# Optimization experiments

Hardware: AMD Instinct MI355X
Metric: run time of the kernel (lower is better)

The kernel has to match this reference:

```python
import jax, jax.numpy as jnp
import numpy as np

N, E, G = 2000, 8000, 100          # nodes, edges, graphs
F_NODE, F_EDGE, H, FC = 22, 4, 128, 64
EPS = 1e-5                          # BatchNorm eps (eval mode, running stats)


def setup_inputs() -> dict:
    key = jax.random.key(0)
    ks = jax.random.split(key, 24)
    rn = lambda k, s, sc=0.1: jax.random.normal(k, s, jnp.float32) * sc
    inp = {}
    inp["x"] = jax.random.normal(ks[0], (N, F_NODE), jnp.float32)
    inp["edge_index"] = jax.random.randint(ks[1], (2, E), 0, N, jnp.int64)
    inp["edge_attr"] = jax.random.uniform(ks[2], (E, F_EDGE), jnp.float32)
    inp["batch"] = jnp.sort(jax.random.randint(ks[3], (N,), 0, G, jnp.int64))
    # edge networks (Linear + ReLU) producing per-edge weight matrices
    inp["We1"] = rn(ks[4], (F_EDGE, F_NODE * H)); inp["be1"] = jnp.zeros((F_NODE * H,), jnp.float32)
    inp["We2"] = rn(ks[5], (F_EDGE, H * H));      inp["be2"] = jnp.zeros((H * H,), jnp.float32)
    inp["We3"] = rn(ks[6], (F_EDGE, H * H));      inp["be3"] = jnp.zeros((H * H,), jnp.float32)
    # NNConv root weights + biases
    inp["Wr1"] = rn(ks[7], (F_NODE, H)); inp["br1"] = jnp.zeros((H,), jnp.float32)
    inp["Wr2"] = rn(ks[8], (H, H));      inp["br2"] = jnp.zeros((H,), jnp.float32)
    inp["Wr3"] = rn(ks[9], (H, H));      inp["br3"] = jnp.zeros((H,), jnp.float32)
    # BatchNorm (eval): gamma, beta, running_mean, running_var
    for i, k in zip((1, 2, 3), (ks[10], ks[11], ks[12])):
        inp[f"g{i}"] = 1.0 + rn(k, (H,), 0.05)
        inp[f"b{i}"] = jnp.zeros((H,), jnp.float32)
        inp[f"rm{i}"] = jnp.zeros((H,), jnp.float32)
        inp[f"rv{i}"] = jnp.ones((H,), jnp.float32)
    # head MLP
    inp["Wf1"] = rn(ks[13], (H, FC)); inp["bf1"] = jnp.zeros((FC,), jnp.float32)
    inp["Wf2"] = rn(ks[14], (FC, 1)); inp["bf2"] = jnp.zeros((1,), jnp.float32)
    return inp


def _nnconv(x, src, dst, edge_attr, We, be, Wr, br, din, dout):
    # per-edge weight matrix from edge features: [E, din, dout]
    w = jax.nn.relu(edge_attr @ We + be).reshape(-1, din, dout)
    msg = jnp.einsum('ei,eio->eo', x[src], w)          # gather + batched matvec
    agg = jax.ops.segment_sum(msg, dst, num_segments=N)  # scatter-add at targets
    return agg + x @ Wr + br                            # root transform + bias


def _bn(x, g, b, rm, rv):
    return (x - rm) * jax.lax.rsqrt(rv + EPS) * g + b


def reference(x, edge_index, edge_attr, batch,
              We1, be1, We2, be2, We3, be3,
              Wr1, br1, Wr2, br2, Wr3, br3,
              g1, b1, rm1, rv1, g2, b2, rm2, rv2, g3, b3, rm3, rv3,
              Wf1, bf1, Wf2, bf2):
    src, dst = edge_index[0], edge_index[1]
    h = jax.nn.relu(_bn(_nnconv(x, src, dst, edge_attr, We1, be1, Wr1, br1, F_NODE, H), g1, b1, rm1, rv1))
    h = jax.nn.relu(_bn(_nnconv(h, src, dst, edge_attr, We2, be2, Wr2, br2, H, H), g2, b2, rm2, rv2))
    h = jax.nn.relu(_bn(_nnconv(h, src, dst, edge_attr, We3, be3, Wr3, br3, H, H), g3, b3, rm3, rv3))
    # global mean pool over graphs
    sums = jax.ops.segment_sum(h, batch, num_segments=G)
    cnts = jax.ops.segment_sum(jnp.ones((N,), h.dtype), batch, num_segments=G)
    pooled = sums / jnp.maximum(cnts, 1.0)[:, None]
    # head MLP (dropout is identity at inference)
    out = jax.nn.relu(pooled @ Wf1 + bf1) @ Wf2 + bf2
    return out  # [G, 1]
```

## Files before the change

### kernel.cpp

```cpp
#include <hip/hip_runtime.h>
#include <hip/hip_bf16.h>
#include <math.h>

#define N_NODES 2000
#define N_EDGES 8000
#define N_GRAPH 100
#define F_NODE 22
#define F_EDGE 4
#define H 128
#define FC 64
#define EPSBN 1e-5f
#define EPB 16
#define EPT 8

#define C2 (H * H)
#define NEB (N_EDGES / EPB)

#define MSG1_B NEB
#define ROOT1_B (N_NODES / 8)
#define PRE_TOTAL (2 * C2 + 2 * 4096 + 3 * H)
#define PRE_B ((PRE_TOTAL + 255) / 256)
#define GRID1 (MSG1_B + ROOT1_B + PRE_B)

#define MSGH_B (NEB * 2)
#define ROOTH_B (N_NODES / 8)
#define GRID23 (MSGH_B + ROOTH_B)


#define COMP_CHUNK(WREG, BREG, BASE)                                           \
  {                                                                            \
    float bu_[4] = {BREG.x, BREG.y, BREG.z, BREG.w};                           \
    _Pragma("unroll")                                                          \
    for (int u = 0; u < 4; u++) {                                              \
      float4 xa_ = *(const float4*)&xs[(BASE) + u][eh * EPT];                  \
      float4 xb_ = *(const float4*)&xs[(BASE) + u][eh * EPT + 4];              \
      float xq_[8] = {xa_.x, xa_.y, xa_.z, xa_.w, xb_.x, xb_.y, xb_.z, xb_.w}; \
      float4 wv_ = WREG[u];                                                    \
      _Pragma("unroll")                                                        \
      for (int q = 0; q < 8; q++) {                                            \
        float w_ = fmaf(wv_.x, ear[q][0], bu_[u]);                             \
        w_ = fmaf(wv_.y, ear[q][1], w_);                                       \
        w_ = fmaf(wv_.z, ear[q][2], w_);                                       \
        w_ = fmaf(wv_.w, ear[q][3], w_);                                       \
        w_ = fmaxf(w_, 0.f);                                                   \
        acc[q] = fmaf(xq_[q], w_, acc[q]);                                     \
      }                                                                        \
    }                                                                          \
  }

__device__ __forceinline__ void msg_body_H(
    const float* __restrict__ xin, const int* __restrict__ ei,
    const float* __restrict__ ea, const float4* __restrict__ Wp,
    const float4* __restrict__ bp4, const float* __restrict__ ABp,
    float* __restrict__ agg, int mblk)
{
    __shared__ float xs[64][EPB];
    __shared__ float eas[EPB][4];
    __shared__ int dsts[EPB];
    const int eb = mblk % NEB;
    const int I0 = (mblk / NEB) * 64;
    const int e0 = eb * EPB;
    const int tid = threadIdx.x;

    if (tid < EPB * 4) { int e = tid >> 2, k = tid & 3; eas[e][k] = ea[(e0 + e) * 4 + k]; }
    if (tid >= 64 && tid < 64 + EPB) dsts[tid - 64] = ei[N_EDGES + e0 + (tid - 64)];
    for (int idx = tid; idx < EPB * 64; idx += 256) {
        int i = idx >> 4, e = idx & 15;
        int s = ei[e0 + e];
        float v = xin[s * H + I0 + i];
        xs[i][e] = fmaxf(fmaf(v, ABp[I0 + i], ABp[H + I0 + i]), 0.f);
    }
    __syncthreads();

    const int o = tid & 127;
    const int eh = tid >> 7;

    float ear[EPT][4], acc[EPT];
#pragma unroll
    for (int q = 0; q < EPT; q++) {
        acc[q] = 0.f;
#pragma unroll
        for (int k = 0; k < 4; k++) ear[q][k] = eas[eh * EPT + q][k];
    }

    const float4* wp = Wp + I0 * H + o;
    const float4* bp = bp4 + (I0 / 4) * H + o;

    float4 wA[4], wB[4], bA, bB;
#pragma unroll
    for (int u = 0; u < 4; u++) wA[u] = wp[u * H];
    bA = bp[0];

#pragma unroll 1
    for (int ii = 0; ii < 64; ii += 8) {
#pragma unroll
        for (int u = 0; u < 4; u++) wB[u] = wp[(ii + 4 + u) * H];
        bB = bp[(ii / 4 + 1) * H];
        COMP_CHUNK(wA, bA, ii)
        if (ii + 8 < 64) {
#pragma unroll
            for (int u = 0; u < 4; u++) wA[u] = wp[(ii + 8 + u) * H];
            bA = bp[(ii / 4 + 2) * H];
        }
        COMP_CHUNK(wB, bB, ii + 4)
    }

#pragma unroll
    for (int q = 0; q < EPT; q++)
        atomicAdd(&agg[dsts[eh * EPT + q] * H + o], acc[q]);
}

__device__ __forceinline__ void msg_body_1(
    const float* __restrict__ xin, const int* __restrict__ ei,
    const float* __restrict__ ea, const float* __restrict__ We1,
    const float* __restrict__ be1, float* __restrict__ agg, int mblk)
{
    __shared__ float xs[24][EPB];
    __shared__ float eas[EPB][4];
    __shared__ int dsts[EPB];
    const int e0 = mblk * EPB;
    const int tid = threadIdx.x;

    if (tid < EPB * 4) { int e = tid >> 2, k = tid & 3; eas[e][k] = ea[(e0 + e) * 4 + k]; }
    if (tid >= 64 && tid < 64 + EPB) dsts[tid - 64] = ei[N_EDGES + e0 + (tid - 64)];
    for (int idx = tid; idx < EPB * 24; idx += 256) {
        int i = idx >> 4, e = idx & 15;
        int s = ei[e0 + e];
        xs[i][e] = (i < F_NODE) ? xin[s * F_NODE + i] : 0.f;
    }
    __syncthreads();

    const int o = tid & 127;
    const int eh = tid >> 7;

    float ear[EPT][4], acc[EPT];
#pragma unroll
    for (int q = 0; q < EPT; q++) {
        acc[q] = 0.f;
#pragma unroll
        for (int k = 0; k < 4; k++) ear[q][k] = eas[eh * EPT + q][k];
    }

    for (int ii = 0; ii < 24; ii += 4) {
        float4 w4[4]; float bb[4];
#pragma unroll
        for (int u = 0; u < 4; u++) {
            int row = ii + u;
            if (row < F_NODE) {
                w4[u] = make_float4(We1[0 * (F_NODE * H) + row * H + o],
                                    We1[1 * (F_NODE * H) + row * H + o],
                                    We1[2 * (F_NODE * H) + row * H + o],
                                    We1[3 * (F_NODE * H) + row * H + o]);
                bb[u] = be1[row * H + o];
            } else { w4[u] = make_float4(0.f, 0.f, 0.f, 0.f); bb[u] = 0.f; }
        }
#pragma unroll
        for (int u = 0; u < 4; u++) {
            float4 xa = *(const float4*)&xs[ii + u][eh * EPT];
            float4 xb = *(const float4*)&xs[ii + u][eh * EPT + 4];
            float xq[8] = {xa.x, xa.y, xa.z, xa.w, xb.x, xb.y, xb.z, xb.w};
            float4 wv = w4[u];
#pragma unroll
            for (int q = 0; q < 8; q++) {
                float w = fmaf(wv.x, ear[q][0], bb[u]);
                w = fmaf(wv.y, ear[q][1], w);
                w = fmaf(wv.z, ear[q][2], w);
                w = fmaf(wv.w, ear[q][3], w);
                w = fmaxf(w, 0.f);
                acc[q] = fmaf(xq[q], w, acc[q]);
            }
        }
    }

#pragma unroll
    for (int q = 0; q < EPT; q++)
        atomicAdd(&agg[dsts[eh * EPT + q] * H + o], acc[q]);
}

template <int DIN, bool ACT>
__device__ __forceinline__ void root_body(
    const float* __restrict__ hin, const float4* __restrict__ Wr4,
    const float4* __restrict__ br4, const float* __restrict__ ABp,
    float* __restrict__ agg, int rblk)
{
    constexpr int NPB = 8;
    __shared__ float hs[NPB][DIN];
    const int n0 = rblk * NPB;
    const int tid = threadIdx.x;
    for (int idx = tid; idx < NPB * DIN; idx += 256) {
        int nl = idx / DIN, i = idx - nl * DIN;
        float v = hin[(n0 + nl) * DIN + i];
        if (ACT) v = fmaxf(fmaf(v, ABp[i], ABp[H + i]), 0.f);
        hs[nl][i] = v;
    }
    __syncthreads();
    const int og = tid & 31;
    const int nl = tid >> 5;
    float4 acc = br4[og];
#pragma unroll 4
    for (int i = 0; i < DIN; i++) {
        float4 w = Wr4[i * (H / 4) + og];
        float xv = hs[nl][i];
        acc.x = fmaf(xv, w.x, acc.x);
        acc.y = fmaf(xv, w.y, acc.y);
        acc.z = fmaf(xv, w.z, acc.z);
        acc.w = fmaf(xv, w.w, acc.w);
    }
    float* dst = agg + (n0 + nl) * H + og * 4;
    atomicAdd(dst + 0, acc.x);
    atomicAdd(dst + 1, acc.y);
    atomicAdd(dst + 2, acc.z);
    atomicAdd(dst + 3, acc.w);
}

__device__ __forceinline__ void pre_body(
    const float* __restrict__ We2, const float* __restrict__ be2,
    const float* __restrict__ We3, const float* __restrict__ be3,
    const float* __restrict__ g1, const float* __restrict__ b1,
    const float* __restrict__ rm1, const float* __restrict__ rv1,
    const float* __restrict__ g2, const float* __restrict__ b2,
    const float* __restrict__ rm2, const float* __restrict__ rv2,
    const float* __restrict__ g3, const float* __restrict__ b3,
    const float* __restrict__ rm3, const float* __restrict__ rv3,
    float4* __restrict__ We2p, float4* __restrict__ We3p,
    float4* __restrict__ be2p4, float4* __restrict__ be3p4,
    float* __restrict__ AB, int pblk)
{
    int t = pblk * 256 + threadIdx.x;
    if (t < C2) {
        We2p[t] = make_float4(We2[t], We2[C2 + t], We2[2 * C2 + t], We2[3 * C2 + t]);
        return;
    }
    t -= C2;
    if (t < C2) {
        We3p[t] = make_float4(We3[t], We3[C2 + t], We3[2 * C2 + t], We3[3 * C2 + t]);
        return;
    }
    t -= C2;
    if (t < 4096) {
        int c = t / H, o = t - c * H;
        be2p4[t] = make_float4(be2[(4 * c) * H + o], be2[(4 * c + 1) * H + o],
                               be2[(4 * c + 2) * H + o], be2[(4 * c + 3) * H + o]);
        return;
    }
    t -= 4096;
    if (t < 4096) {
        int c = t / H, o = t - c * H;
        be3p4[t] = make_float4(be3[(4 * c) * H + o], be3[(4 * c + 1) * H + o],
                               be3[(4 * c + 2) * H + o], be3[(4 * c + 3) * H + o]);
        return;
    }
    t -= 4096;
    if (t < 3 * H) {
        int l = t / H, o = t - l * H;
        const float *g, *b, *rm, *rv;
        if (l == 0) { g = g1; b = b1; rm = rm1; rv = rv1; }
        else if (l == 1) { g = g2; b = b2; rm = rm2; rv = rv2; }
        else { g = g3; b = b3; rm = rm3; rv = rv3; }
        float A = g[o] * rsqrtf(rv[o] + EPSBN);
        AB[l * 2 * H + o] = A;
        AB[l * 2 * H + H + o] = b[o] - rm[o] * A;
    }
}

__global__ __launch_bounds__(256) void stage1_kernel(
    const float* x, const int* ei, const float* ea,
    const float* We1, const float* be1,
    const float4* Wr1_4, const float4* br1_4,
    const float* We2, const float* be2, const float* We3, const float* be3,
    const float* g1, const float* b1, const float* rm1, const float* rv1,
    const float* g2, const float* b2, const float* rm2, const float* rv2,
    const float* g3, const float* b3, const float* rm3, const float* rv3,
    float4* We2p, float4* We3p, float4* be2p4, float4* be3p4, float* AB,
    float* h1)
{
    const int b = blockIdx.x;
    if (b < MSG1_B) {
        msg_body_1(x, ei, ea, We1, be1, h1, b);
    } else if (b < MSG1_B + ROOT1_B) {
        root_body<F_NODE, false>(x, Wr1_4, br1_4, nullptr, h1, b - MSG1_B);
    } else {
        pre_body(We2, be2, We3, be3,
                 g1, b1, rm1, rv1, g2, b2, rm2, rv2, g3, b3, rm3, rv3,
                 We2p, We3p, be2p4, be3p4, AB, b - MSG1_B - ROOT1_B);
    }
}

__global__ __launch_bounds__(256) void layer_kernel(
    const float* hin, const int* ei, const float* ea,
    const float4* Wp, const float4* bp4,
    const float4* Wr4, const float4* br4,
    const float* ABprev, float* hout)
{
    const int b = blockIdx.x;
    if (b < MSGH_B) {
        msg_body_H(hin, ei, ea, Wp, bp4, ABprev, hout, b);
    } else {
        root_body<H, true>(hin, Wr4, br4, ABprev, hout, b - MSGH_B);
    }
}

__global__ __launch_bounds__(128) void pool_head_kernel(
    const float* __restrict__ h, const int* __restrict__ batch,
    const float* __restrict__ AB,
    const float* __restrict__ Wf1, const float* __restrict__ bf1,
    const float* __restrict__ Wf2, const float* __restrict__ bf2,
    float* __restrict__ out)
{
    __shared__ float pooled[H];
    const int g = blockIdx.x;
    const int t = threadIdx.x;

    int a = 0, b = N_NODES;
    while (a < b) { int m = (a + b) >> 1; if (batch[m] < g) a = m + 1; else b = m; }
    const int lo = a;
    b = N_NODES;
    while (a < b) { int m = (a + b) >> 1; if (batch[m] < g + 1) a = m + 1; else b = m; }
    const int hi = a;

    float s = 0.f;
    const float Ao = AB[t], Bo = AB[H + t];
    for (int n = lo; n < hi; n++) {
        float v = h[n * H + t];
        s += fmaxf(fmaf(v, Ao, Bo), 0.f);
    }
    pooled[t] = (hi > lo) ? s / (float)(hi - lo) : 0.f;
    __syncthreads();

    if (t < FC) {
        float f = bf1[t];
#pragma unroll 4
        for (int i = 0; i < H; i++) f = fmaf(pooled[i], Wf1[i * FC + t], f);
        f = fmaxf(f, 0.f);
        float p = f * Wf2[t];
#pragma unroll
        for (int off = 32; off; off >>= 1) p += __shfl_down(p, off);
        if (t == 0) out[g] = p + bf2[0];
    }
}

extern "C" void kernel_launch(void* const* d_in, const int* in_sizes, int n_in,
                              void* d_out, int out_size, void* d_ws, size_t ws_size,
                              hipStream_t stream) {
    const float* x   = (const float*)d_in[0];
    const int* ei    = (const int*)d_in[1];
    const float* ea  = (const float*)d_in[2];
    const int* batch = (const int*)d_in[3];
    const float* We1 = (const float*)d_in[4];
    const float* be1 = (const float*)d_in[5];
    const float* We2 = (const float*)d_in[6];
    const float* be2 = (const float*)d_in[7];
    const float* We3 = (const float*)d_in[8];
    const float* be3 = (const float*)d_in[9];
    const float* Wr1 = (const float*)d_in[10];
    const float* br1 = (const float*)d_in[11];
    const float* Wr2 = (const float*)d_in[12];
    const float* br2 = (const float*)d_in[13];
    const float* Wr3 = (const float*)d_in[14];
    const float* br3 = (const float*)d_in[15];
    const float* g1 = (const float*)d_in[16], *b1 = (const float*)d_in[17];
    const float* rm1 = (const float*)d_in[18], *rv1 = (const float*)d_in[19];
    const float* g2 = (const float*)d_in[20], *b2 = (const float*)d_in[21];
    const float* rm2 = (const float*)d_in[22], *rv2 = (const float*)d_in[23];
    const float* g3 = (const float*)d_in[24], *b3 = (const float*)d_in[25];
    const float* rm3 = (const float*)d_in[26], *rv3 = (const float*)d_in[27];
    const float* Wf1 = (const float*)d_in[28];
    const float* bf1 = (const float*)d_in[29];
    const float* Wf2 = (const float*)d_in[30];
    const float* bf2 = (const float*)d_in[31];

    float* out = (float*)d_out;

    float* ws = (float*)d_ws;
    float* h1    = ws;
    float* h2    = h1 + N_NODES * H;
    float* h3    = h2 + N_NODES * H;
    float* We2p  = h3 + N_NODES * H;
    float* We3p  = We2p + C2 * 4;
    float* be2p4 = We3p + C2 * 4;
    float* be3p4 = be2p4 + 4096 * 4;
    float* AB    = be3p4 + 4096 * 4;

    stage1_kernel<<<GRID1, 256, 0, stream>>>(
        x, ei, ea, We1, be1,
        (const float4*)Wr1, (const float4*)br1,
        We2, be2, We3, be3,
        g1, b1, rm1, rv1, g2, b2, rm2, rv2, g3, b3, rm3, rv3,
        (float4*)We2p, (float4*)We3p, (float4*)be2p4, (float4*)be3p4, AB,
        h1);

    layer_kernel<<<GRID23, 256, 0, stream>>>(
        h1, ei, ea, (const float4*)We2p, (const float4*)be2p4,
        (const float4*)Wr2, (const float4*)br2, AB + 0 * 2 * H, h2);

    layer_kernel<<<GRID23, 256, 0, stream>>>(
        h2, ei, ea, (const float4*)We3p, (const float4*)be3p4,
        (const float4*)Wr3, (const float4*)br3, AB + 1 * 2 * H, h3);

    pool_head_kernel<<<N_GRAPH, 128, 0, stream>>>(
        h3, batch, AB + 2 * 2 * H, Wf1, bf1, Wf2, bf2, out);
}
```

Baseline: 200.3 us.

## Fuse all stages into one cooperative persistent kernel with grid syncs

Replaces the four sequential kernel launches with a single cooperative persistent kernel that loops over work units per phase and separates phases with grid-wide syncs. The goal is to remove launch overhead and inter-kernel gaps, which are significant for a workload of only a few hundred microseconds. The grid is capped by occupancy times CU count, so blocks may process several units in series. The per-call host occupancy and attribute queries add CPU overhead, and a fallback path keeps the old multi-kernel launch sequence.

```diff
diff --git a/kernel.cpp b/kernel.cpp
--- a/kernel.cpp
+++ b/kernel.cpp
@@ -1,6 +1,9 @@
 #include <hip/hip_runtime.h>
+#include <hip/hip_cooperative_groups.h>
 #include <hip/hip_bf16.h>
 #include <math.h>
+
+namespace cg = cooperative_groups;
 
 #define N_NODES 2000
 #define N_EDGES 8000
@@ -20,11 +23,11 @@
 #define ROOT1_B (N_NODES / 8)
 #define PRE_TOTAL (2 * C2 + 2 * 4096 + 3 * H)
 #define PRE_B ((PRE_TOTAL + 255) / 256)
-#define GRID1 (MSG1_B + ROOT1_B + PRE_B)
+#define PHA_U (MSG1_B + ROOT1_B + PRE_B)
 
 #define MSGH_B (NEB * 2)
 #define ROOTH_B (N_NODES / 8)
-#define GRID23 (MSGH_B + ROOTH_B)
+#define PHB_U (MSGH_B + ROOTH_B)
 
 
 #define COMP_CHUNK(WREG, BREG, BASE)                                           \
@@ -115,18 +118,18 @@
     const float* __restrict__ ea, const float* __restrict__ We1,
     const float* __restrict__ be1, float* __restrict__ agg, int mblk)
 {
-    __shared__ float xs[24][EPB];
-    __shared__ float eas[EPB][4];
-    __shared__ int dsts[EPB];
+    __shared__ float xs1[24][EPB];
+    __shared__ float eas1[EPB][4];
+    __shared__ int dsts1[EPB];
     const int e0 = mblk * EPB;
     const int tid = threadIdx.x;
 
-    if (tid < EPB * 4) { int e = tid >> 2, k = tid & 3; eas[e][k] = ea[(e0 + e) * 4 + k]; }
-    if (tid >= 64 && tid < 64 + EPB) dsts[tid - 64] = ei[N_EDGES + e0 + (tid - 64)];
+    if (tid < EPB * 4) { int e = tid >> 2, k = tid & 3; eas1[e][k] = ea[(e0 + e) * 4 + k]; }
+    if (tid >= 64 && tid < 64 + EPB) dsts1[tid - 64] = ei[N_EDGES + e0 + (tid - 64)];
     for (int idx = tid; idx < EPB * 24; idx += 256) {
         int i = idx >> 4, e = idx & 15;
         int s = ei[e0 + e];
-        xs[i][e] = (i < F_NODE) ? xin[s * F_NODE + i] : 0.f;
+        xs1[i][e] = (i < F_NODE) ? xin[s * F_NODE + i] : 0.f;
     }
     __syncthreads();
 
@@ -138,7 +141,7 @@
     for (int q = 0; q < EPT; q++) {
         acc[q] = 0.f;
 #pragma unroll
-        for (int k = 0; k < 4; k++) ear[q][k] = eas[eh * EPT + q][k];
+        for (int k = 0; k < 4; k++) ear[q][k] = eas1[eh * EPT + q][k];
     }
 
     for (int ii = 0; ii < 24; ii += 4) {
@@ -156,8 +159,8 @@
         }
 #pragma unroll
         for (int u = 0; u < 4; u++) {
-            float4 xa = *(const float4*)&xs[ii + u][eh * EPT];
-            float4 xb = *(const float4*)&xs[ii + u][eh * EPT + 4];
+            float4 xa = *(const float4*)&xs1[ii + u][eh * EPT];
+            float4 xb = *(const float4*)&xs1[ii + u][eh * EPT + 4];
             float xq[8] = {xa.x, xa.y, xa.z, xa.w, xb.x, xb.y, xb.z, xb.w};
             float4 wv = w4[u];
 #pragma unroll
@@ -174,7 +177,7 @@
 
 #pragma unroll
     for (int q = 0; q < EPT; q++)
-        atomicAdd(&agg[dsts[eh * EPT + q] * H + o], acc[q]);
+        atomicAdd(&agg[dsts1[eh * EPT + q] * H + o], acc[q]);
 }
 
 template <int DIN, bool ACT>
@@ -263,52 +266,14 @@
     }
 }
 
-__global__ __launch_bounds__(256) void stage1_kernel(
-    const float* x, const int* ei, const float* ea,
-    const float* We1, const float* be1,
-    const float4* Wr1_4, const float4* br1_4,
-    const float* We2, const float* be2, const float* We3, const float* be3,
-    const float* g1, const float* b1, const float* rm1, const float* rv1,
-    const float* g2, const float* b2, const float* rm2, const float* rv2,
-    const float* g3, const float* b3, const float* rm3, const float* rv3,
-    float4* We2p, float4* We3p, float4* be2p4, float4* be3p4, float* AB,
-    float* h1)
-{
-    const int b = blockIdx.x;
-    if (b < MSG1_B) {
-        msg_body_1(x, ei, ea, We1, be1, h1, b);
-    } else if (b < MSG1_B + ROOT1_B) {
-        root_body<F_NODE, false>(x, Wr1_4, br1_4, nullptr, h1, b - MSG1_B);
-    } else {
-        pre_body(We2, be2, We3, be3,
-                 g1, b1, rm1, rv1, g2, b2, rm2, rv2, g3, b3, rm3, rv3,
-                 We2p, We3p, be2p4, be3p4, AB, b - MSG1_B - ROOT1_B);
-    }
-}
-
-__global__ __launch_bounds__(256) void layer_kernel(
-    const float* hin, const int* ei, const float* ea,
-    const float4* Wp, const float4* bp4,
-    const float4* Wr4, const float4* br4,
-    const float* ABprev, float* hout)
-{
-    const int b = blockIdx.x;
-    if (b < MSGH_B) {
-        msg_body_H(hin, ei, ea, Wp, bp4, ABprev, hout, b);
-    } else {
-        root_body<H, true>(hin, Wr4, br4, ABprev, hout, b - MSGH_B);
-    }
-}
-
-__global__ __launch_bounds__(128) void pool_head_kernel(
+__device__ __forceinline__ void pool_head_body(
     const float* __restrict__ h, const int* __restrict__ batch,
     const float* __restrict__ AB,
     const float* __restrict__ Wf1, const float* __restrict__ bf1,
     const float* __restrict__ Wf2, const float* __restrict__ bf2,
-    float* __restrict__ out)
+    float* __restrict__ out, int g)
 {
     __shared__ float pooled[H];
-    const int g = blockIdx.x;
     const int t = threadIdx.x;
 
     int a = 0, b = N_NODES;
@@ -318,13 +283,15 @@
     while (a < b) { int m = (a + b) >> 1; if (batch[m] < g + 1) a = m + 1; else b = m; }
     const int hi = a;
 
-    float s = 0.f;
-    const float Ao = AB[t], Bo = AB[H + t];
-    for (int n = lo; n < hi; n++) {
-        float v = h[n * H + t];
-        s += fmaxf(fmaf(v, Ao, Bo), 0.f);
-    }
-    pooled[t] = (hi > lo) ? s / (float)(hi - lo) : 0.f;
+    if (t < H) {
+        float s = 0.f;
+        const float Ao = AB[t], Bo = AB[H + t];
+        for (int n = lo; n < hi; n++) {
+            float v = h[n * H + t];
+            s += fmaxf(fmaf(v, Ao, Bo), 0.f);
+        }
+        pooled[t] = (hi > lo) ? s / (float)(hi - lo) : 0.f;
+    }
     __syncthreads();
 
     if (t < FC) {
@@ -339,38 +306,119 @@
     }
 }
 
+struct KArgs {
+    const float *x; const int *ei; const float *ea; const int *batch;
+    const float *We1, *be1, *We2, *be2, *We3, *be3;
+    const float *Wr1, *br1, *Wr2, *br2, *Wr3, *br3;
+    const float *g1, *b1, *rm1, *rv1;
+    const float *g2, *b2, *rm2, *rv2;
+    const float *g3, *b3, *rm3, *rv3;
+    const float *Wf1, *bf1, *Wf2, *bf2;
+    float *out;
+    float *h1, *h2, *h3, *We2p, *We3p, *be2p4, *be3p4, *AB;
+};
+
+__global__ __launch_bounds__(256) void mpnn_kernel(KArgs a)
+{
+    cg::grid_group grid = cg::this_grid();
+    const int G = gridDim.x;
+
+    for (int u = blockIdx.x; u < PHA_U; u += G) {
+        if (u < MSG1_B) {
+            msg_body_1(a.x, a.ei, a.ea, a.We1, a.be1, a.h1, u);
+        } else if (u < MSG1_B + ROOT1_B) {
+            root_body<F_NODE, false>(a.x, (const float4*)a.Wr1, (const float4*)a.br1,
+                                     nullptr, a.h1, u - MSG1_B);
+        } else {
+            pre_body(a.We2, a.be2, a.We3, a.be3,
+                     a.g1, a.b1, a.rm1, a.rv1, a.g2, a.b2, a.rm2, a.rv2,
+                     a.g3, a.b3, a.rm3, a.rv3,
+                     (float4*)a.We2p, (float4*)a.We3p,
+                     (float4*)a.be2p4, (float4*)a.be3p4, a.AB,
+                     u - MSG1_B - ROOT1_B);
+        }
+        __syncthreads();
+    }
+    grid.sync();
+
+    for (int u = blockIdx.x; u < PHB_U; u += G) {
+        if (u < MSGH_B)
+            msg_body_H(a.h1, a.ei, a.ea, (const float4*)a.We2p,
+                       (const float4*)a.be2p4, a.AB + 0 * 2 * H, a.h2, u);
+        else
+            root_body<H, true>(a.h1, (const float4*)a.Wr2, (const float4*)a.br2,
+                               a.AB + 0 * 2 * H, a.h2, u - MSGH_B);
+        __syncthreads();
+    }
+    grid.sync();
+
+    for (int u = blockIdx.x; u < PHB_U; u += G) {
+        if (u < MSGH_B)
+            msg_body_H(a.h2, a.ei, a.ea, (const float4*)a.We3p,
+                       (const float4*)a.be3p4, a.AB + 1 * 2 * H, a.h3, u);
+        else
+            root_body<H, true>(a.h2, (const float4*)a.Wr3, (const float4*)a.br3,
+                               a.AB + 1 * 2 * H, a.h3, u - MSGH_B);
+        __syncthreads();
+    }
+    grid.sync();
+
+    for (int u = blockIdx.x; u < N_GRAPH; u += G) {
+        pool_head_body(a.h3, a.batch, a.AB + 2 * 2 * H,
+                       a.Wf1, a.bf1, a.Wf2, a.bf2, a.out, u);
+        __syncthreads();
+    }
+}
+
+__global__ __launch_bounds__(256) void stage1_kernel(KArgs a)
+{
+    const int b = blockIdx.x;
+    if (b < MSG1_B) {
+        msg_body_1(a.x, a.ei, a.ea, a.We1, a.be1, a.h1, b);
+    } else if (b < MSG1_B + ROOT1_B) {
+        root_body<F_NODE, false>(a.x, (const float4*)a.Wr1, (const float4*)a.br1,
+                                 nullptr, a.h1, b - MSG1_B);
+    } else {
+        pre_body(a.We2, a.be2, a.We3, a.be3,
+                 a.g1, a.b1, a.rm1, a.rv1, a.g2, a.b2, a.rm2, a.rv2,
+                 a.g3, a.b3, a.rm3, a.rv3,
+                 (float4*)a.We2p, (float4*)a.We3p,
+                 (float4*)a.be2p4, (float4*)a.be3p4, a.AB,
+                 b - MSG1_B - ROOT1_B);
+    }
+}
+
+__global__ __launch_bounds__(256) void layer2_kernel(KArgs a)
+{
+    const int b = blockIdx.x;
+    if (b < MSGH_B)
+        msg_body_H(a.h1, a.ei, a.ea, (const float4*)a.We2p,
+                   (const float4*)a.be2p4, a.AB + 0 * 2 * H, a.h2, b);
+    else
+        root_body<H, true>(a.h1, (const float4*)a.Wr2, (const float4*)a.br2,
+                           a.AB + 0 * 2 * H, a.h2, b - MSGH_B);
+}
+
+__global__ __launch_bounds__(256) void layer3_kernel(KArgs a)
+{
+    const int b = blockIdx.x;
+    if (b < MSGH_B)
+        msg_body_H(a.h2, a.ei, a.ea, (const float4*)a.We3p,
+                   (const float4*)a.be3p4, a.AB + 1 * 2 * H, a.h3, b);
+    else
+        root_body<H, true>(a.h2, (const float4*)a.Wr3, (const float4*)a.br3,
+                           a.AB + 1 * 2 * H, a.h3, b - MSGH_B);
+}
+
+__global__ __launch_bounds__(128) void pool_head_kernel(KArgs a)
+{
+    pool_head_body(a.h3, a.batch, a.AB + 2 * 2 * H,
+                   a.Wf1, a.bf1, a.Wf2, a.bf2, a.out, blockIdx.x);
+}
+
 extern "C" void kernel_launch(void* const* d_in, const int* in_sizes, int n_in,
                               void* d_out, int out_size, void* d_ws, size_t ws_size,
                               hipStream_t stream) {
-    const float* x   = (const float*)d_in[0];
-    const int* ei    = (const int*)d_in[1];
-    const float* ea  = (const float*)d_in[2];
-    const int* batch = (const int*)d_in[3];
-    const float* We1 = (const float*)d_in[4];
-    const float* be1 = (const float*)d_in[5];
-    const float* We2 = (const float*)d_in[6];
-    const float* be2 = (const float*)d_in[7];
-    const float* We3 = (const float*)d_in[8];
-    const float* be3 = (const float*)d_in[9];
-    const float* Wr1 = (const float*)d_in[10];
-    const float* br1 = (const float*)d_in[11];
-    const float* Wr2 = (const float*)d_in[12];
-    const float* br2 = (const float*)d_in[13];
-    const float* Wr3 = (const float*)d_in[14];
-    const float* br3 = (const float*)d_in[15];
-    const float* g1 = (const float*)d_in[16], *b1 = (const float*)d_in[17];
-    const float* rm1 = (const float*)d_in[18], *rv1 = (const float*)d_in[19];
-    const float* g2 = (const float*)d_in[20], *b2 = (const float*)d_in[21];
-    const float* rm2 = (const float*)d_in[22], *rv2 = (const float*)d_in[23];
-    const float* g3 = (const float*)d_in[24], *b3 = (const float*)d_in[25];
-    const float* rm3 = (const float*)d_in[26], *rv3 = (const float*)d_in[27];
-    const float* Wf1 = (const float*)d_in[28];
-    const float* bf1 = (const float*)d_in[29];
-    const float* Wf2 = (const float*)d_in[30];
-    const float* bf2 = (const float*)d_in[31];
-
-    float* out = (float*)d_out;
-
     float* ws = (float*)d_ws;
     float* h1    = ws;
     float* h2    = h1 + N_NODES * H;
@@ -381,22 +429,48 @@
     float* be3p4 = be2p4 + 4096 * 4;
     float* AB    = be3p4 + 4096 * 4;
 
-    stage1_kernel<<<GRID1, 256, 0, stream>>>(
-        x, ei, ea, We1, be1,
-        (const float4*)Wr1, (const float4*)br1,
-        We2, be2, We3, be3,
-        g1, b1, rm1, rv1, g2, b2, rm2, rv2, g3, b3, rm3, rv3,
-        (float4*)We2p, (float4*)We3p, (float4*)be2p4, (float4*)be3p4, AB,
-        h1);
-
-    layer_kernel<<<GRID23, 256, 0, stream>>>(
-        h1, ei, ea, (const float4*)We2p, (const float4*)be2p4,
-        (const float4*)Wr2, (const float4*)br2, AB + 0 * 2 * H, h2);
-
-    layer_kernel<<<GRID23, 256, 0, stream>>>(
-        h2, ei, ea, (const float4*)We3p, (const float4*)be3p4,
-        (const float4*)Wr3, (const float4*)br3, AB + 1 * 2 * H, h3);
-
-    pool_head_kernel<<<N_GRAPH, 128, 0, stream>>>(
-        h3, batch, AB + 2 * 2 * H, Wf1, bf1, Wf2, bf2, out);
-}
+    KArgs a;
+    a.x   = (const float*)d_in[0];
+    a.ei  = (const int*)d_in[1];
+    a.ea  = (const float*)d_in[2];
+    a.batch = (const int*)d_in[3];
+    a.We1 = (const float*)d_in[4];  a.be1 = (const float*)d_in[5];
+    a.We2 = (const float*)d_in[6];  a.be2 = (const float*)d_in[7];
+    a.We3 = (const float*)d_in[8];  a.be3 = (const float*)d_in[9];
+    a.Wr1 = (const float*)d_in[10]; a.br1 = (const float*)d_in[11];
+    a.Wr2 = (const float*)d_in[12]; a.br2 = (const float*)d_in[13];
+    a.Wr3 = (const float*)d_in[14]; a.br3 = (const float*)d_in[15];
+    a.g1 = (const float*)d_in[16]; a.b1 = (const float*)d_in[17];
+    a.rm1 = (const float*)d_in[18]; a.rv1 = (const float*)d_in[19];
+    a.g2 = (const float*)d_in[20]; a.b2 = (const float*)d_in[21];
+    a.rm2 = (const float*)d_in[22]; a.rv2 = (const float*)d_in[23];
+    a.g3 = (const float*)d_in[24]; a.b3 = (const float*)d_in[25];
+    a.rm3 = (const float*)d_in[26]; a.rv3 = (const float*)d_in[27];
+    a.Wf1 = (const float*)d_in[28]; a.bf1 = (const float*)d_in[29];
+    a.Wf2 = (const float*)d_in[30]; a.bf2 = (const float*)d_in[31];
+    a.out = (float*)d_out;
+    a.h1 = h1; a.h2 = h2; a.h3 = h3;
+    a.We2p = We2p; a.We3p = We3p; a.be2p4 = be2p4; a.be3p4 = be3p4; a.AB = AB;
+
+    int coop = 0, numCU = 0, maxB = 0, dev = 0;
+    hipGetDevice(&dev);
+    hipDeviceGetAttribute(&coop, hipDeviceAttributeCooperativeLaunch, dev);
+    hipDeviceGetAttribute(&numCU, hipDeviceAttributeMultiprocessorCount, dev);
+    hipOccupancyMaxActiveBlocksPerMultiprocessor(&maxB, mpnn_kernel, 256, 0);
+
+    if (coop && maxB > 0 && numCU > 0) {
+        int grid = maxB * numCU;
+        if (grid > PHB_U) grid = PHB_U;
+        void* kargs[] = { (void*)&a };
+        hipError_t err = hipLaunchCooperativeKernel((const void*)mpnn_kernel,
+                                                    dim3(grid), dim3(256),
+                                                    kargs, 0, stream);
+        if (err == hipSuccess) return;
+        (void)hipGetLastError();
+    }
+
+    stage1_kernel<<<PHA_U, 256, 0, stream>>>(a);
+    layer2_kernel<<<PHB_U, 256, 0, stream>>>(a);
+    layer3_kernel<<<PHB_U, 256, 0, stream>>>(a);
+    pool_head_kernel<<<N_GRAPH, 128, 0, stream>>>(a);
+}
```

Measured after the change: 377.1 us. +88.2%, slower.
